# Kernel optimization log

Measured on AMD Instinct MI355X. Metric: run time of the kernel, lower is better.

## Reference

```python
import jax, jax.numpy as jnp
import numpy as np


def setup_inputs() -> dict:
    key = jax.random.key(0)
    ks = jax.random.split(key, 6)
    B, Cx, Cf, Ch, H, W = 4, 512, 512, 256, 64, 64
    return {
        "query_features": jax.random.normal(ks[0], (B, Cx, H, W), dtype=jnp.float32),
        "reference_features": jax.random.normal(ks[1], (B, Cf, H, W), dtype=jnp.float32),
        "Wq": jax.random.normal(ks[2], (Ch, Cx), dtype=jnp.float32) * (1.0 / np.sqrt(Cx)),
        "bq": jax.random.normal(ks[3], (Ch,), dtype=jnp.float32) * 0.02,
        "Wk": jax.random.normal(ks[4], (Ch, Cf), dtype=jnp.float32) * (1.0 / np.sqrt(Cf)),
        "bk": jax.random.normal(ks[5], (Ch,), dtype=jnp.float32) * 0.02,
    }


def reference(query_features, reference_features, Wq, bq, Wk, bk):
    # 1x1 convs == per-pixel linear projections over channels
    Q = jnp.einsum('bchw,oc->bohw', query_features, Wq) + bq[None, :, None, None]
    K = jnp.einsum('bchw,oc->bohw', reference_features, Wk) + bk[None, :, None, None]
    B, Cf, H2, W2 = reference_features.shape
    H1, W1 = Q.shape[2], Q.shape[3]
    V = reference_features.reshape(B, Cf, H2 * W2)            # b c p
    # unscaled QK^T over hidden channels: [b, h1, w1, h2*w2]
    scores = jnp.einsum('bcij,bckl->bijkl', Q, K).reshape(B, H1, W1, H2 * W2)
    attn = jax.nn.softmax(scores, axis=-1)
    out = jnp.einsum('bijp,bcp->bcij', attn, V)               # [b, Cf, h1, w1]
    return out
```

## Files before the change

### kernel.cpp

```cpp
#include <hip/hip_runtime.h>
#include <hip/hip_bf16.h>
#include <hip/hip_fp16.h>

typedef _Float16 half8 __attribute__((ext_vector_type(8)));
typedef _Float16 half4v __attribute__((ext_vector_type(4)));
typedef float f4 __attribute__((ext_vector_type(4)));
typedef float f16v __attribute__((ext_vector_type(16)));
typedef short short8 __attribute__((ext_vector_type(8)));
typedef unsigned short us8 __attribute__((ext_vector_type(8)));
typedef int i4 __attribute__((ext_vector_type(4)));

#define P_SZ 4096
#define CH 256
#define CIN 512
#define CV 512
#define KVB 32
#define L2E 1.4426950408889634f

__device__ __forceinline__ unsigned short f2bf(float f) {
  unsigned u = __float_as_uint(f);
  unsigned r = u + 0x7fffu + ((u >> 16) & 1u);
  return (unsigned short)(r >> 16);
}
__device__ __forceinline__ float bf2f(unsigned short h) {
  return __uint_as_float(((unsigned)h) << 16);
}

__device__ __forceinline__ void gload16(const void* g, void* l) {
  __builtin_amdgcn_global_load_lds(
      (const __attribute__((address_space(1))) unsigned int*)g,
      (__attribute__((address_space(3))) unsigned int*)l, 16, 0, 0);
}

__global__ __launch_bounds__(256) void wconv_kernel(
    const float* __restrict__ Wq, const float* __restrict__ Wk,
    short* __restrict__ Wh, short* __restrict__ Wl) {
  const int i = blockIdx.x * 256 + threadIdx.x;
  const int which = i >> 17;
  const int j = i & 131071;
  const float w = which ? Wk[j] : Wq[j] * L2E;
  const unsigned short h = f2bf(w);
  Wh[i] = (short)h;
  Wl[i] = (short)f2bf(w - bf2f(h));
}

__global__ __launch_bounds__(256) void vconv_kernel(const float* __restrict__ in,
                                                    _Float16* __restrict__ outv) {
  __shared__ _Float16 T[512][34];
  const int b = blockIdx.x >> 7;
  const int tile = blockIdx.x & 127;
  const int tid = threadIdx.x;
  const float* src = in + (size_t)b * CIN * P_SZ + tile * 32;
  const int c0 = tid >> 3, j4 = tid & 7;
  #pragma unroll
  for (int pass = 0; pass < 16; ++pass) {
    const int c = pass * 32 + c0;
    const f4 x = *(const f4*)(src + (size_t)c * P_SZ + j4 * 4);
    half4v h;
    h[0] = (_Float16)x[0]; h[1] = (_Float16)x[1];
    h[2] = (_Float16)x[2]; h[3] = (_Float16)x[3];
    *(half4v*)&T[c][j4 * 4] = h;
  }
  __syncthreads();
  _Float16* dst = outv + (size_t)b * 2097152 + (size_t)tile * 16384;
  #pragma unroll
  for (int i = 0; i < 8; ++i) {
    const int kh = i >> 1;
    const int ch = ((i & 1) << 8) + tid;
    *(half8*)(dst + kh * 4096 + ch * 8) = *(const half8*)&T[ch][kh * 8];
  }
}

__global__ __launch_bounds__(512) void proj_kernel(
    const float* __restrict__ Xq, const float* __restrict__ bq,
    const float* __restrict__ Xk, const float* __restrict__ bk,
    const short* __restrict__ Wh, const short* __restrict__ Wl,
    _Float16* __restrict__ Qout, _Float16* __restrict__ Kout) {
  __shared__ float Xs[64][65];
  const int which = blockIdx.z;
  const float* __restrict__ X = which ? Xk : Xq;
  const float* __restrict__ bias = which ? bk : bq;
  _Float16* __restrict__ out = which ? Kout : Qout;
  const float bscale = which ? 1.f : L2E;

  const int b = blockIdx.y;
  const int p0 = blockIdx.x * 64;
  const int tid = threadIdx.x;
  const int w = tid >> 6, l = tid & 63;
  const int wp = w >> 2, wo = w & 3;
  const int lr = l & 15, lg = l >> 4;

  const float* __restrict__ Xb = X + (size_t)b * CIN * P_SZ;
  const short* __restrict__ Whb = Wh + (size_t)which * 131072;
  const short* __restrict__ Wlb = Wl + (size_t)which * 131072;

  f4 acc[2][4];
  #pragma unroll
  for (int m = 0; m < 2; ++m)
    #pragma unroll
    for (int n = 0; n < 4; ++n) acc[m][n] = (f4){0.f, 0.f, 0.f, 0.f};

  const int crow = tid >> 4;
  const int pq4 = (tid & 15) * 4;

  #pragma unroll 1
  for (int kc64 = 0; kc64 < CIN; kc64 += 64) {
    __syncthreads();
    #pragma unroll
    for (int h2 = 0; h2 < 2; ++h2) {
      const int c = crow + h2 * 32;
      const f4 x = *(const f4*)(Xb + (size_t)(kc64 + c) * P_SZ + p0 + pq4);
      Xs[pq4 + 0][c] = x[0];
      Xs[pq4 + 1][c] = x[1];
      Xs[pq4 + 2][c] = x[2];
      Xs[pq4 + 3][c] = x[3];
    }
    __syncthreads();

    #pragma unroll
    for (int s = 0; s < 2; ++s) {
      const int kc = kc64 + s * 32;
      short8 ah[2], al[2];
      #pragma unroll
      for (int m = 0; m < 2; ++m) {
        const int pl = wp * 32 + m * 16 + lr;
        #pragma unroll
        for (int i = 0; i < 8; ++i) {
          float xv = Xs[pl][s * 32 + lg * 8 + i];
          unsigned short h = f2bf(xv);
          ah[m][i] = (short)h;
          al[m][i] = (short)f2bf(xv - bf2f(h));
        }
      }
      short8 bh[4], bl[4];
      #pragma unroll
      for (int n = 0; n < 4; ++n) {
        const size_t wi = (size_t)(wo * 64 + n * 16 + lr) * CIN + kc + lg * 8;
        bh[n] = *(const short8*)(Whb + wi);
        bl[n] = *(const short8*)(Wlb + wi);
      }
      #pragma unroll
      for (int m = 0; m < 2; ++m)
        #pragma unroll
        for (int n = 0; n < 4; ++n) {
          acc[m][n] = __builtin_amdgcn_mfma_f32_16x16x32_bf16(ah[m], bh[n], acc[m][n], 0, 0, 0);
          acc[m][n] = __builtin_amdgcn_mfma_f32_16x16x32_bf16(ah[m], bl[n], acc[m][n], 0, 0, 0);
          acc[m][n] = __builtin_amdgcn_mfma_f32_16x16x32_bf16(al[m], bh[n], acc[m][n], 0, 0, 0);
        }
    }
  }

  #pragma unroll
  for (int n = 0; n < 4; ++n) {
    const int o = wo * 64 + n * 16 + lr;
    const float bv = bias[o] * bscale;
    #pragma unroll
    for (int m = 0; m < 2; ++m) {
      #pragma unroll
      for (int j = 0; j < 4; ++j) {
        const int p = p0 + wp * 32 + m * 16 + lg * 4 + j;
        const _Float16 val = (_Float16)(acc[m][n][j] + bv);
        if (which == 0) {
          out[((size_t)b * P_SZ + p) * CH + o] = val;
        } else {
          const int kk = p & 31;
          const int kswz = (kk & 19) | ((kk & 4) << 1) | ((kk & 8) >> 1);
          out[(size_t)b * 1048576 + (size_t)(p >> 5) * 8192
              + (size_t)(o >> 3) * 256 + kswz * 8 + (o & 7)] = val;
        }
      }
    }
  }
}

template <int NSEG, bool DIRECT>
__global__ __launch_bounds__(512, 2) void attn_kernel(
    const _Float16* __restrict__ Qg, const _Float16* __restrict__ Kt,
    const _Float16* __restrict__ Vt, unsigned short* __restrict__ Opart,
    float* __restrict__ Mp, float* __restrict__ Lp, float* __restrict__ Og) {
  __shared__ char K_l[3][16384];
  __shared__ char V_l[3][32768];

  constexpr int nt = (P_SZ / NSEG) / KVB;
  int b, qt, seg;
  if (NSEG == 2) {
    const int g = blockIdx.x & 7;
    b = g >> 1; seg = g & 1; qt = blockIdx.x >> 3;
  } else {
    b = blockIdx.x & 3; seg = 0; qt = blockIdx.x >> 2;
  }

  const int tid = threadIdx.x;
  const int w = tid >> 6, l = tid & 63;
  const int hi = l >> 5, l31 = l & 31;
  const int wq = w >> 1, half = w & 1;

  const char* Kb = (const char*)Kt + (size_t)b * 2097152 + (size_t)seg * nt * 16384;
  const char* Vb = (const char*)Vt + (size_t)b * 4194304 + (size_t)seg * nt * 32768;

#define STAGE(BUF, T) do { \
    const char* ksrc = Kb + (size_t)(T) * 16384; \
    const char* vsrc = Vb + (size_t)(T) * 32768; \
    gload16(ksrc + tid * 16,         &K_l[BUF][w * 1024]); \
    gload16(ksrc + 8192 + tid * 16,  &K_l[BUF][8192 + w * 1024]); \
    gload16(vsrc + tid * 16,         &V_l[BUF][w * 1024]); \
    gload16(vsrc + 8192 + tid * 16,  &V_l[BUF][8192 + w * 1024]); \
    gload16(vsrc + 16384 + tid * 16, &V_l[BUF][16384 + w * 1024]); \
    gload16(vsrc + 24576 + tid * 16, &V_l[BUF][24576 + w * 1024]); \
  } while (0)

  half8 qf[16];
  {
    const char* qrow = (const char*)Qg +
        ((size_t)b * P_SZ + qt * 128 + wq * 32 + l31) * 512;
    #pragma unroll
    for (int m = 0; m < 16; ++m) qf[m] = *(const half8*)(qrow + m * 32 + hi * 16);
  }

  f16v acc[8];
  #pragma unroll
  for (int n = 0; n < 8; ++n)
    acc[n] = (f16v){0,0,0,0, 0,0,0,0, 0,0,0,0, 0,0,0,0};

  float m_run = -1e30f, lsum = 0.f;
  const int kread = hi * 512 + l31 * 16;
  const int vread = hi * 8192 + half * 4096 + l31 * 16;

  STAGE(0, 0); STAGE(1, 1);
  asm volatile("s_waitcnt vmcnt(6)" ::: "memory");
  asm volatile("s_barrier" ::: "memory");

  int bufc = 0;
  #pragma unroll 1
  for (int t = 0; t < nt; ++t) {
    const char* kb = &K_l[bufc][0] + kread;
    f16v s = (f16v){0,0,0,0, 0,0,0,0, 0,0,0,0, 0,0,0,0};
    __builtin_amdgcn_s_setprio(1);
    #pragma unroll
    for (int m = 0; m < 16; ++m) {
      half8 kf = *(const half8*)(kb + m * 1024);
      s = __builtin_amdgcn_mfma_f32_32x32x16_f16(kf, qf[m], s, 0, 0, 0);
    }
    __builtin_amdgcn_s_setprio(0);

    float x0 = fmaxf(s[0], s[8]),  x1 = fmaxf(s[1], s[9]);
    float x2 = fmaxf(s[2], s[10]), x3 = fmaxf(s[3], s[11]);
    float x4 = fmaxf(s[4], s[12]), x5 = fmaxf(s[5], s[13]);
    float x6 = fmaxf(s[6], s[14]), x7 = fmaxf(s[7], s[15]);
    x0 = fmaxf(x0, x4); x1 = fmaxf(x1, x5); x2 = fmaxf(x2, x6); x3 = fmaxf(x3, x7);
    float pm = fmaxf(fmaxf(x0, x1), fmaxf(x2, x3));
    pm = fmaxf(pm, __shfl_xor(pm, 32));
    if (__any(pm > m_run + 12.f)) {
      const float mnew = fmaxf(m_run, pm);
      const float al = __builtin_amdgcn_exp2f(m_run - mnew);
      const int alb = __float_as_int(al);
      #pragma unroll
      for (int r = 0; r < 16; ++r) {
        const int cr = (r & 3) + 8 * (r >> 2);
        const float ar = __int_as_float(
            __builtin_amdgcn_ds_bpermute(cr * 4 + hi * 16, alb));
        #pragma unroll
        for (int n = 0; n < 8; ++n) acc[n][r] *= ar;
      }
      lsum *= al;
      m_run = mnew;
    }
    float p[16], psum;
    #pragma unroll
    for (int r = 0; r < 16; ++r) p[r] = __builtin_amdgcn_exp2f(s[r] - m_run);
    {
      float a0 = (p[0] + p[1]) + (p[2] + p[3]);
      float a1 = (p[4] + p[5]) + (p[6] + p[7]);
      float a2 = (p[8] + p[9]) + (p[10] + p[11]);
      float a3 = (p[12] + p[13]) + (p[14] + p[15]);
      psum = (a0 + a1) + (a2 + a3);
      psum += __shfl_xor(psum, 32);
    }
    lsum += psum;

    i4 w0v, w1v;
    w0v[0] = __builtin_bit_cast(int, __builtin_amdgcn_cvt_pkrtz(p[0], p[1]));
    w0v[1] = __builtin_bit_cast(int, __builtin_amdgcn_cvt_pkrtz(p[2], p[3]));
    w0v[2] = __builtin_bit_cast(int, __builtin_amdgcn_cvt_pkrtz(p[4], p[5]));
    w0v[3] = __builtin_bit_cast(int, __builtin_amdgcn_cvt_pkrtz(p[6], p[7]));
    w1v[0] = __builtin_bit_cast(int, __builtin_amdgcn_cvt_pkrtz(p[8], p[9]));
    w1v[1] = __builtin_bit_cast(int, __builtin_amdgcn_cvt_pkrtz(p[10], p[11]));
    w1v[2] = __builtin_bit_cast(int, __builtin_amdgcn_cvt_pkrtz(p[12], p[13]));
    w1v[3] = __builtin_bit_cast(int, __builtin_amdgcn_cvt_pkrtz(p[14], p[15]));
    const half8 pa0 = __builtin_bit_cast(half8, w0v);
    const half8 pa1 = __builtin_bit_cast(half8, w1v);

    const int bufs = bufc == 0 ? 2 : bufc - 1;
    if (t + 2 < nt) STAGE(bufs, t + 2);

    const char* vb = &V_l[bufc][0] + vread;
    __builtin_amdgcn_s_setprio(1);
    #pragma unroll
    for (int n = 0; n < 8; ++n) {
      half8 v0 = *(const half8*)(vb + n * 512);
      acc[n] = __builtin_amdgcn_mfma_f32_32x32x16_f16(pa0, v0, acc[n], 0, 0, 0);
      half8 v1 = *(const half8*)(vb + 16384 + n * 512);
      acc[n] = __builtin_amdgcn_mfma_f32_32x32x16_f16(pa1, v1, acc[n], 0, 0, 0);
    }
    __builtin_amdgcn_s_setprio(0);

    if (t + 2 < nt) { asm volatile("s_waitcnt vmcnt(6)" ::: "memory"); }
    else            { asm volatile("s_waitcnt vmcnt(0)" ::: "memory"); }
    asm volatile("s_barrier" ::: "memory");
    bufc = bufc == 2 ? 0 : bufc + 1;
  }
#undef STAGE

  const int qg0 = qt * 128 + wq * 32;
  if (!DIRECT) {
    unsigned short* Ob = Opart +
        (((size_t)seg * 4 + b) * P_SZ + qg0) * 512 + half * 256 + l31;
    #pragma unroll
    for (int n = 0; n < 8; ++n) {
      #pragma unroll
      for (int r = 0; r < 16; ++r) {
        const int q = (r & 3) + 8 * (r >> 2) + 4 * hi;
        Ob[(size_t)q * 512 + n * 32] = f2bf(acc[n][r]);
      }
    }
    if (half == 0 && l < 32) {
      const size_t mi = ((size_t)seg * 4 + b) * P_SZ + qg0 + l31;
      Mp[mi] = m_run; Lp[mi] = lsum;
    }
  } else {
    float linv[16];
    const int lb = __float_as_int(lsum);
    #pragma unroll
    for (int r = 0; r < 16; ++r) {
      const int cr = (r & 3) + 8 * (r >> 2);
      const float lq = __int_as_float(__builtin_amdgcn_ds_bpermute(cr * 4 + hi * 16, lb));
      linv[r] = 1.f / lq;
    }
    #pragma unroll
    for (int n = 0; n < 8; ++n) {
      #pragma unroll
      for (int r = 0; r < 16; ++r) {
        const int q = (r & 3) + 8 * (r >> 2) + 4 * hi;
        Og[((size_t)b * CV + half * 256 + n * 32 + l31) * P_SZ + qg0 + q] =
            acc[n][r] * linv[r];
      }
    }
  }
}

template <int NSEG>
__global__ __launch_bounds__(256) void combine_kernel(
    const unsigned short* __restrict__ Opart, const float* __restrict__ Mp,
    const float* __restrict__ Lp, float* __restrict__ Og) {
  __shared__ float T[64][65];
  const int bx = blockIdx.x;
  const int ct = bx & 7, qt = (bx >> 3) & 63, b = bx >> 9;
  const int tid = threadIdx.x;
  {
    const int qi = tid >> 2, cj = tid & 3;
    const int q = qt * 64 + qi;
    const size_t mibase = (size_t)b * P_SZ + q;
    float M = -1e30f;
    #pragma unroll
    for (int s = 0; s < NSEG; ++s) M = fmaxf(M, Mp[(size_t)s * 4 * P_SZ + mibase]);
    float L = 0.f;
    float o[16];
    #pragma unroll
    for (int e = 0; e < 16; ++e) o[e] = 0.f;
    #pragma unroll
    for (int s = 0; s < NSEG; ++s) {
      const float wgt = __builtin_amdgcn_exp2f(Mp[(size_t)s * 4 * P_SZ + mibase] - M);
      L += wgt * Lp[(size_t)s * 4 * P_SZ + mibase];
      const unsigned short* src = Opart +
          (((size_t)s * 4 + b) * P_SZ + q) * 512 + ct * 64 + cj * 16;
      const us8 ua = ((const us8*)src)[0];
      const us8 ub = ((const us8*)src)[1];
      #pragma unroll
      for (int e = 0; e < 8; ++e) {
        o[e]     += wgt * bf2f(ua[e]);
        o[8 + e] += wgt * bf2f(ub[e]);
      }
    }
    const float inv = 1.f / L;
    #pragma unroll
    for (int e = 0; e < 16; ++e) T[qi][cj * 16 + e] = o[e] * inv;
  }
  __syncthreads();
  const int ci = tid >> 2, qj = tid & 3;
  #pragma unroll
  for (int i = 0; i < 4; ++i) {
    f4 v;
    #pragma unroll
    for (int e = 0; e < 4; ++e) v[e] = T[qj * 16 + i * 4 + e][ci];
    *(f4*)&Og[((size_t)b * CV + ct * 64 + ci) * P_SZ + qt * 64 + qj * 16 + i * 4] = v;
  }
}

extern "C" void kernel_launch(void* const* d_in, const int* in_sizes, int n_in,
                              void* d_out, int out_size, void* d_ws, size_t ws_size,
                              hipStream_t stream) {
  const float* x  = (const float*)d_in[0];
  const float* f  = (const float*)d_in[1];
  const float* Wq = (const float*)d_in[2];
  const float* bq = (const float*)d_in[3];
  const float* Wk = (const float*)d_in[4];
  const float* bk = (const float*)d_in[5];
  float* out = (float*)d_out;

  char* ws = (char*)d_ws;
  _Float16* Qf = (_Float16*)ws;
  _Float16* Kf = (_Float16*)(ws + ((size_t)8 << 20));
  _Float16* Vf = (_Float16*)(ws + ((size_t)16 << 20));
  float* Mp    = (float*)(ws + ((size_t)32 << 20));
  float* Lp    = (float*)(ws + ((size_t)32 << 20) + (256 << 10));
  short* Wh    = (short*)(ws + ((size_t)32 << 20) + (512 << 10));
  short* Wl    = (short*)(ws + ((size_t)33 << 20));
  unsigned short* Opart = (unsigned short*)(ws + ((size_t)34 << 20));

  wconv_kernel<<<dim3(1024), dim3(256), 0, stream>>>(Wq, Wk, Wh, Wl);
  vconv_kernel<<<dim3(512), dim3(256), 0, stream>>>(f, Vf);
  proj_kernel<<<dim3(64, 4, 2), dim3(512), 0, stream>>>(x, bq, f, bk, Wh, Wl, Qf, Kf);

  const size_t need2 = ((size_t)34 << 20) + ((size_t)32 << 20);
  const size_t need1 = ((size_t)34 << 20) + ((size_t)16 << 20);
  if (ws_size >= need2) {
    attn_kernel<2, false><<<dim3(256), dim3(512), 0, stream>>>(Qf, Kf, Vf, Opart, Mp, Lp, nullptr);
    combine_kernel<2><<<dim3(2048), dim3(256), 0, stream>>>(Opart, Mp, Lp, out);
  } else if (ws_size >= need1) {
    attn_kernel<1, false><<<dim3(128), dim3(512), 0, stream>>>(Qf, Kf, Vf, Opart, Mp, Lp, nullptr);
    combine_kernel<1><<<dim3(2048), dim3(256), 0, stream>>>(Opart, Mp, Lp, out);
  } else {
    attn_kernel<1, true><<<dim3(128), dim3(512), 0, stream>>>(Qf, Kf, Vf, nullptr, nullptr, nullptr, out);
  }
}
```

Baseline: 262.4 us.

## Double KV tile to 64 keys with double-buffered K and single-buffered V

The attention loop now processes 64 keys per iteration instead of 32. K tiles are double-buffered and prefetched one iteration ahead, while V uses a single 64 KB buffer that is loaded at the start of each iteration and waited on before the PV MFMAs. The projection kernel writes K in a matching 64-key swizzled layout. The aim is to halve the barrier count and cut LDS usage, at the cost of a shallower V prefetch: V load latency is now hidden only by the current tile's QK compute.

```diff
diff --git a/kernel.cpp b/kernel.cpp
--- a/kernel.cpp
+++ b/kernel.cpp
@@ -14,7 +14,6 @@
 #define CH 256
 #define CIN 512
 #define CV 512
-#define KVB 32
 #define L2E 1.4426950408889634f
 
 __device__ __forceinline__ unsigned short f2bf(float f) {
@@ -165,8 +164,8 @@
         } else {
           const int kk = p & 31;
           const int kswz = (kk & 19) | ((kk & 4) << 1) | ((kk & 8) >> 1);
-          out[(size_t)b * 1048576 + (size_t)(p >> 5) * 8192
-              + (size_t)(o >> 3) * 256 + kswz * 8 + (o & 7)] = val;
+          out[(size_t)b * 1048576 + (size_t)(p >> 6) * 16384
+              + (size_t)(o >> 3) * 512 + ((p >> 5) & 1) * 256 + kswz * 8 + (o & 7)] = val;
         }
       }
     }
@@ -178,10 +177,10 @@
     const _Float16* __restrict__ Qg, const _Float16* __restrict__ Kt,
     const _Float16* __restrict__ Vt, unsigned short* __restrict__ Opart,
     float* __restrict__ Mp, float* __restrict__ Lp, float* __restrict__ Og) {
-  __shared__ char K_l[3][16384];
-  __shared__ char V_l[3][32768];
-
-  constexpr int nt = (P_SZ / NSEG) / KVB;
+  __shared__ char K_l[2][32768];
+  __shared__ char V_l[65536];
+
+  constexpr int nt = (P_SZ / NSEG) / 64;
   int b, qt, seg;
   if (NSEG == 2) {
     const int g = blockIdx.x & 7;
@@ -195,18 +194,26 @@
   const int hi = l >> 5, l31 = l & 31;
   const int wq = w >> 1, half = w & 1;
 
-  const char* Kb = (const char*)Kt + (size_t)b * 2097152 + (size_t)seg * nt * 16384;
-  const char* Vb = (const char*)Vt + (size_t)b * 4194304 + (size_t)seg * nt * 32768;
-
-#define STAGE(BUF, T) do { \
-    const char* ksrc = Kb + (size_t)(T) * 16384; \
-    const char* vsrc = Vb + (size_t)(T) * 32768; \
-    gload16(ksrc + tid * 16,         &K_l[BUF][w * 1024]); \
-    gload16(ksrc + 8192 + tid * 16,  &K_l[BUF][8192 + w * 1024]); \
-    gload16(vsrc + tid * 16,         &V_l[BUF][w * 1024]); \
-    gload16(vsrc + 8192 + tid * 16,  &V_l[BUF][8192 + w * 1024]); \
-    gload16(vsrc + 16384 + tid * 16, &V_l[BUF][16384 + w * 1024]); \
-    gload16(vsrc + 24576 + tid * 16, &V_l[BUF][24576 + w * 1024]); \
+  const char* Kb = (const char*)Kt + (size_t)b * 2097152 + (size_t)seg * nt * 32768;
+  const char* Vb = (const char*)Vt + (size_t)b * 4194304 + (size_t)seg * nt * 65536;
+
+#define STAGE_K(BUF, T) do { \
+    const char* ksrc = Kb + (size_t)(T) * 32768; \
+    gload16(ksrc + tid * 16,          &K_l[BUF][w * 1024]); \
+    gload16(ksrc + 8192 + tid * 16,   &K_l[BUF][8192 + w * 1024]); \
+    gload16(ksrc + 16384 + tid * 16,  &K_l[BUF][16384 + w * 1024]); \
+    gload16(ksrc + 24576 + tid * 16,  &K_l[BUF][24576 + w * 1024]); \
+  } while (0)
+#define STAGE_V(T) do { \
+    const char* vsrc = Vb + (size_t)(T) * 65536; \
+    gload16(vsrc + tid * 16,          &V_l[w * 1024]); \
+    gload16(vsrc + 8192 + tid * 16,   &V_l[8192 + w * 1024]); \
+    gload16(vsrc + 16384 + tid * 16,  &V_l[16384 + w * 1024]); \
+    gload16(vsrc + 24576 + tid * 16,  &V_l[24576 + w * 1024]); \
+    gload16(vsrc + 32768 + tid * 16,  &V_l[32768 + w * 1024]); \
+    gload16(vsrc + 40960 + tid * 16,  &V_l[40960 + w * 1024]); \
+    gload16(vsrc + 49152 + tid * 16,  &V_l[49152 + w * 1024]); \
+    gload16(vsrc + 57344 + tid * 16,  &V_l[57344 + w * 1024]); \
   } while (0)
 
   half8 qf[16];
@@ -223,93 +230,100 @@
     acc[n] = (f16v){0,0,0,0, 0,0,0,0, 0,0,0,0, 0,0,0,0};
 
   float m_run = -1e30f, lsum = 0.f;
-  const int kread = hi * 512 + l31 * 16;
+  const int kread = hi * 1024 + l31 * 16;
   const int vread = hi * 8192 + half * 4096 + l31 * 16;
 
-  STAGE(0, 0); STAGE(1, 1);
-  asm volatile("s_waitcnt vmcnt(6)" ::: "memory");
+  STAGE_K(0, 0);
+  asm volatile("s_waitcnt vmcnt(0)" ::: "memory");
   asm volatile("s_barrier" ::: "memory");
 
-  int bufc = 0;
   #pragma unroll 1
   for (int t = 0; t < nt; ++t) {
-    const char* kb = &K_l[bufc][0] + kread;
-    f16v s = (f16v){0,0,0,0, 0,0,0,0, 0,0,0,0, 0,0,0,0};
-    __builtin_amdgcn_s_setprio(1);
-    #pragma unroll
-    for (int m = 0; m < 16; ++m) {
-      half8 kf = *(const half8*)(kb + m * 1024);
-      s = __builtin_amdgcn_mfma_f32_32x32x16_f16(kf, qf[m], s, 0, 0, 0);
-    }
-    __builtin_amdgcn_s_setprio(0);
-
-    float x0 = fmaxf(s[0], s[8]),  x1 = fmaxf(s[1], s[9]);
-    float x2 = fmaxf(s[2], s[10]), x3 = fmaxf(s[3], s[11]);
-    float x4 = fmaxf(s[4], s[12]), x5 = fmaxf(s[5], s[13]);
-    float x6 = fmaxf(s[6], s[14]), x7 = fmaxf(s[7], s[15]);
-    x0 = fmaxf(x0, x4); x1 = fmaxf(x1, x5); x2 = fmaxf(x2, x6); x3 = fmaxf(x3, x7);
-    float pm = fmaxf(fmaxf(x0, x1), fmaxf(x2, x3));
-    pm = fmaxf(pm, __shfl_xor(pm, 32));
-    if (__any(pm > m_run + 12.f)) {
-      const float mnew = fmaxf(m_run, pm);
-      const float al = __builtin_amdgcn_exp2f(m_run - mnew);
-      const int alb = __float_as_int(al);
-      #pragma unroll
-      for (int r = 0; r < 16; ++r) {
-        const int cr = (r & 3) + 8 * (r >> 2);
-        const float ar = __int_as_float(
-            __builtin_amdgcn_ds_bpermute(cr * 4 + hi * 16, alb));
+    STAGE_V(t);
+    if (t + 1 < nt) STAGE_K((t + 1) & 1, t + 1);
+
+    const char* kb = &K_l[t & 1][0] + kread;
+
+    #pragma unroll
+    for (int ksub = 0; ksub < 2; ++ksub) {
+      f16v s = (f16v){0,0,0,0, 0,0,0,0, 0,0,0,0, 0,0,0,0};
+      __builtin_amdgcn_s_setprio(1);
+      #pragma unroll
+      for (int m = 0; m < 16; ++m) {
+        half8 kf = *(const half8*)(kb + m * 2048 + ksub * 512);
+        s = __builtin_amdgcn_mfma_f32_32x32x16_f16(kf, qf[m], s, 0, 0, 0);
+      }
+      __builtin_amdgcn_s_setprio(0);
+
+      float x0 = fmaxf(s[0], s[8]),  x1 = fmaxf(s[1], s[9]);
+      float x2 = fmaxf(s[2], s[10]), x3 = fmaxf(s[3], s[11]);
+      float x4 = fmaxf(s[4], s[12]), x5 = fmaxf(s[5], s[13]);
+      float x6 = fmaxf(s[6], s[14]), x7 = fmaxf(s[7], s[15]);
+      x0 = fmaxf(x0, x4); x1 = fmaxf(x1, x5); x2 = fmaxf(x2, x6); x3 = fmaxf(x3, x7);
+      float pm = fmaxf(fmaxf(x0, x1), fmaxf(x2, x3));
+      pm = fmaxf(pm, __shfl_xor(pm, 32));
+      if (__any(pm > m_run + 12.f)) {
+        const float mnew = fmaxf(m_run, pm);
+        const float al = __builtin_amdgcn_exp2f(m_run - mnew);
+        const int alb = __float_as_int(al);
         #pragma unroll
-        for (int n = 0; n < 8; ++n) acc[n][r] *= ar;
-      }
-      lsum *= al;
-      m_run = mnew;
-    }
-    float p[16], psum;
-    #pragma unroll
-    for (int r = 0; r < 16; ++r) p[r] = __builtin_amdgcn_exp2f(s[r] - m_run);
-    {
-      float a0 = (p[0] + p[1]) + (p[2] + p[3]);
-      float a1 = (p[4] + p[5]) + (p[6] + p[7]);
-      float a2 = (p[8] + p[9]) + (p[10] + p[11]);
-      float a3 = (p[12] + p[13]) + (p[14] + p[15]);
-      psum = (a0 + a1) + (a2 + a3);
-      psum += __shfl_xor(psum, 32);
-    }
-    lsum += psum;
-
-    i4 w0v, w1v;
-    w0v[0] = __builtin_bit_cast(int, __builtin_amdgcn_cvt_pkrtz(p[0], p[1]));
-    w0v[1] = __builtin_bit_cast(int, __builtin_amdgcn_cvt_pkrtz(p[2], p[3]));
-    w0v[2] = __builtin_bit_cast(int, __builtin_amdgcn_cvt_pkrtz(p[4], p[5]));
-    w0v[3] = __builtin_bit_cast(int, __builtin_amdgcn_cvt_pkrtz(p[6], p[7]));
-    w1v[0] = __builtin_bit_cast(int, __builtin_amdgcn_cvt_pkrtz(p[8], p[9]));
-    w1v[1] = __builtin_bit_cast(int, __builtin_amdgcn_cvt_pkrtz(p[10], p[11]));
-    w1v[2] = __builtin_bit_cast(int, __builtin_amdgcn_cvt_pkrtz(p[12], p[13]));
-    w1v[3] = __builtin_bit_cast(int, __builtin_amdgcn_cvt_pkrtz(p[14], p[15]));
-    const half8 pa0 = __builtin_bit_cast(half8, w0v);
-    const half8 pa1 = __builtin_bit_cast(half8, w1v);
-
-    const int bufs = bufc == 0 ? 2 : bufc - 1;
-    if (t + 2 < nt) STAGE(bufs, t + 2);
-
-    const char* vb = &V_l[bufc][0] + vread;
-    __builtin_amdgcn_s_setprio(1);
-    #pragma unroll
-    for (int n = 0; n < 8; ++n) {
-      half8 v0 = *(const half8*)(vb + n * 512);
-      acc[n] = __builtin_amdgcn_mfma_f32_32x32x16_f16(pa0, v0, acc[n], 0, 0, 0);
-      half8 v1 = *(const half8*)(vb + 16384 + n * 512);
-      acc[n] = __builtin_amdgcn_mfma_f32_32x32x16_f16(pa1, v1, acc[n], 0, 0, 0);
-    }
-    __builtin_amdgcn_s_setprio(0);
-
-    if (t + 2 < nt) { asm volatile("s_waitcnt vmcnt(6)" ::: "memory"); }
-    else            { asm volatile("s_waitcnt vmcnt(0)" ::: "memory"); }
+        for (int r = 0; r < 16; ++r) {
+          const int cr = (r & 3) + 8 * (r >> 2);
+          const float ar = __int_as_float(
+              __builtin_amdgcn_ds_bpermute(cr * 4 + hi * 16, alb));
+          #pragma unroll
+          for (int n = 0; n < 8; ++n) acc[n][r] *= ar;
+        }
+        lsum *= al;
+        m_run = mnew;
+      }
+      float p[16], psum;
+      #pragma unroll
+      for (int r = 0; r < 16; ++r) p[r] = __builtin_amdgcn_exp2f(s[r] - m_run);
+      {
+        float a0 = (p[0] + p[1]) + (p[2] + p[3]);
+        float a1 = (p[4] + p[5]) + (p[6] + p[7]);
+        float a2 = (p[8] + p[9]) + (p[10] + p[11]);
+        float a3 = (p[12] + p[13]) + (p[14] + p[15]);
+        psum = (a0 + a1) + (a2 + a3);
+        psum += __shfl_xor(psum, 32);
+      }
+      lsum += psum;
+
+      i4 w0v, w1v;
+      w0v[0] = __builtin_bit_cast(int, __builtin_amdgcn_cvt_pkrtz(p[0], p[1]));
+      w0v[1] = __builtin_bit_cast(int, __builtin_amdgcn_cvt_pkrtz(p[2], p[3]));
+      w0v[2] = __builtin_bit_cast(int, __builtin_amdgcn_cvt_pkrtz(p[4], p[5]));
+      w0v[3] = __builtin_bit_cast(int, __builtin_amdgcn_cvt_pkrtz(p[6], p[7]));
+      w1v[0] = __builtin_bit_cast(int, __builtin_amdgcn_cvt_pkrtz(p[8], p[9]));
+      w1v[1] = __builtin_bit_cast(int, __builtin_amdgcn_cvt_pkrtz(p[10], p[11]));
+      w1v[2] = __builtin_bit_cast(int, __builtin_amdgcn_cvt_pkrtz(p[12], p[13]));
+      w1v[3] = __builtin_bit_cast(int, __builtin_amdgcn_cvt_pkrtz(p[14], p[15]));
+      const half8 pa0 = __builtin_bit_cast(half8, w0v);
+      const half8 pa1 = __builtin_bit_cast(half8, w1v);
+
+      if (ksub == 0) {
+        if (t + 1 < nt) { asm volatile("s_waitcnt vmcnt(4)" ::: "memory"); }
+        else            { asm volatile("s_waitcnt vmcnt(0)" ::: "memory"); }
+      }
+
+      const char* vb = &V_l[ksub * 32768] + vread;
+      __builtin_amdgcn_s_setprio(1);
+      #pragma unroll
+      for (int n = 0; n < 8; ++n) {
+        half8 v0 = *(const half8*)(vb + n * 512);
+        acc[n] = __builtin_amdgcn_mfma_f32_32x32x16_f16(pa0, v0, acc[n], 0, 0, 0);
+        half8 v1 = *(const half8*)(vb + 16384 + n * 512);
+        acc[n] = __builtin_amdgcn_mfma_f32_32x32x16_f16(pa1, v1, acc[n], 0, 0, 0);
+      }
+      __builtin_amdgcn_s_setprio(0);
+    }
+
+    asm volatile("s_waitcnt vmcnt(0)" ::: "memory");
     asm volatile("s_barrier" ::: "memory");
-    bufc = bufc == 2 ? 0 : bufc + 1;
-  }
-#undef STAGE
+  }
+#undef STAGE_K
+#undef STAGE_V
 
   const int qg0 = qt * 128 + wq * 32;
   if (!DIRECT) {
```

New measurement: 263.2 us. No clear change (+0.3%).
